# Kernel optimization log

Hardware: AMD Instinct MI355X
Metric: run time of the kernel (lower is better)

Reference implementation:

```python
import jax, jax.numpy as jnp
import numpy as np


def setup_inputs() -> dict:
    key = jax.random.key(0)
    k1, k2 = jax.random.split(key)
    B, L, D = 8, 4096, 1024
    hidden = jax.random.normal(k1, (B, L, D), dtype=jnp.float32)
    w1 = jax.random.normal(k2, (D // 2 + 1,), dtype=jnp.float32)
    return {"hidden": hidden, "w1": w1}


def reference(hidden, w1):
    # hidden: [B, L, D]; w1: [D//2+1]
    B, L, D = hidden.shape
    flat = hidden.reshape(-1, D)                 # [B*L, D]
    Xf1 = jnp.fft.rfft(flat, axis=1)             # [B*L, D//2+1] complex
    gate = jax.nn.softmax(w1, axis=0)[None, :]   # [1, D//2+1]
    t1 = jnp.fft.irfft(Xf1 * gate, n=D, axis=1)  # [B*L, D]
    return t1.reshape(B, L, D).astype(hidden.dtype)
```

## Files before the change

kernel.cpp:

```cpp
#include <hip/hip_runtime.h>


#define D_N 1024
#define TWO_PI_OVER_N 6.1359231515426636e-03f

__device__ __forceinline__ void cmulf(float& xr, float& xi, float wr, float wi) {
    float r = xr * wr - xi * wi;
    float i = xr * wi + xi * wr;
    xr = r; xi = i;
}

template <int S, bool INV>
__device__ __forceinline__ void fft_stage_store(
    int t,
    float ar, float ai, float br, float bi,
    float cr, float ci, float dr, float di,
    float* __restrict__ yr, float* __restrict__ yi)
{
    float apcr = ar + cr, apci = ai + ci;
    float amcr = ar - cr, amci = ai - ci;
    float bpdr = br + dr, bpdi = bi + di;
    float bmdr = br - dr, bmdi = bi - di;

    float y0r = apcr + bpdr, y0i = apci + bpdi;
    float y2r = apcr - bpdr, y2i = apci - bpdi;
    float y1r, y1i, y3r, y3i;
    if (!INV) {
        y1r = amcr + bmdi; y1i = amci - bmdr;
        y3r = amcr - bmdi; y3i = amci + bmdr;
    } else {
        y1r = amcr - bmdi; y1i = amci + bmdr;
        y3r = amcr + bmdi; y3i = amci - bmdr;
    }

    if (S < 256) {
        int j = t & ~(S - 1);
        float ang = (float)j * TWO_PI_OVER_N;
        float sn, cs;
        __sincosf(ang, &sn, &cs);
        float w1r = cs, w1i = INV ? sn : -sn;
        float w2r = w1r * w1r - w1i * w1i, w2i = 2.0f * w1r * w1i;
        float w3r = w2r * w1r - w2i * w1i, w3i = w2r * w1i + w2i * w1r;
        cmulf(y1r, y1i, w1r, w1i);
        cmulf(y2r, y2i, w2r, w2i);
        cmulf(y3r, y3i, w3r, w3i);
    }

    int bw = (t & (S - 1)) + ((t & ~(S - 1)) << 2);
    yr[bw        ] = y0r; yi[bw        ] = y0i;
    yr[bw +     S] = y1r; yi[bw +     S] = y1i;
    yr[bw + 2 * S] = y2r; yi[bw + 2 * S] = y2i;
    yr[bw + 3 * S] = y3r; yi[bw + 3 * S] = y3i;
}

__global__ __launch_bounds__(256)
void fft_filter_kernel(const float* __restrict__ x,
                       const float* __restrict__ G,
                       float* __restrict__ out)
{
    __shared__ float lAr[D_N], lAi[D_N], lBr[D_N], lBi[D_N];
    const int t = threadIdx.x;
    const size_t base = (size_t)blockIdx.x * D_N;

    {
        float x0 = x[base + t];
        float x1 = x[base + t + 256];
        float x2 = x[base + t + 512];
        float x3 = x[base + t + 768];
        fft_stage_store<1, false>(t, x0, 0.f, x1, 0.f, x2, 0.f, x3, 0.f, lBr, lBi);
    }
    __syncthreads();
    fft_stage_store<4, false>(t,
        lBr[t], lBi[t], lBr[t + 256], lBi[t + 256],
        lBr[t + 512], lBi[t + 512], lBr[t + 768], lBi[t + 768], lAr, lAi);
    __syncthreads();
    fft_stage_store<16, false>(t,
        lAr[t], lAi[t], lAr[t + 256], lAi[t + 256],
        lAr[t + 512], lAi[t + 512], lAr[t + 768], lAi[t + 768], lBr, lBi);
    __syncthreads();
    fft_stage_store<64, false>(t,
        lBr[t], lBi[t], lBr[t + 256], lBi[t + 256],
        lBr[t + 512], lBi[t + 512], lBr[t + 768], lBi[t + 768], lAr, lAi);
    __syncthreads();
    fft_stage_store<256, false>(t,
        lAr[t], lAi[t], lAr[t + 256], lAi[t + 256],
        lAr[t + 512], lAi[t + 512], lAr[t + 768], lAi[t + 768], lBr, lBi);
    __syncthreads();

    {
        float g0 = G[t], g1 = G[t + 256], g2 = G[t + 512], g3 = G[t + 768];
        fft_stage_store<1, true>(t,
            lBr[t] * g0, lBi[t] * g0,
            lBr[t + 256] * g1, lBi[t + 256] * g1,
            lBr[t + 512] * g2, lBi[t + 512] * g2,
            lBr[t + 768] * g3, lBi[t + 768] * g3, lAr, lAi);
    }
    __syncthreads();
    fft_stage_store<4, true>(t,
        lAr[t], lAi[t], lAr[t + 256], lAi[t + 256],
        lAr[t + 512], lAi[t + 512], lAr[t + 768], lAi[t + 768], lBr, lBi);
    __syncthreads();
    fft_stage_store<16, true>(t,
        lBr[t], lBi[t], lBr[t + 256], lBi[t + 256],
        lBr[t + 512], lBi[t + 512], lBr[t + 768], lBi[t + 768], lAr, lAi);
    __syncthreads();
    fft_stage_store<64, true>(t,
        lAr[t], lAi[t], lAr[t + 256], lAi[t + 256],
        lAr[t + 512], lAi[t + 512], lAr[t + 768], lAi[t + 768], lBr, lBi);
    __syncthreads();
    {
        float ar = lBr[t],       ai = lBi[t];
        float br = lBr[t + 256], bi = lBi[t + 256];
        float cr = lBr[t + 512], ci = lBi[t + 512];
        float dr = lBr[t + 768], di = lBi[t + 768];
        float apcr = ar + cr, amcr = ar - cr;
        float bpdr = br + dr, bmdi = bi - di;
        (void)ai; (void)ci;
        float y0r = apcr + bpdr;
        float y2r = apcr - bpdr;
        float y1r = amcr - bmdi;
        float y3r = amcr + bmdi;
        out[base + t      ] = y0r;
        out[base + t + 256] = y1r;
        out[base + t + 512] = y2r;
        out[base + t + 768] = y3r;
    }
}

__global__ void gate_kernel(const float* __restrict__ w1, float* __restrict__ G)
{
    __shared__ float red[1024];
    __shared__ float ex[513];
    const int t = threadIdx.x;

    float v = (t < 513) ? w1[t] : -1e30f;
    red[t] = v;
    __syncthreads();
    for (int off = 512; off > 0; off >>= 1) {
        if (t < off) red[t] = fmaxf(red[t], red[t + off]);
        __syncthreads();
    }
    float M = red[0];
    __syncthreads();

    float e = (t < 513) ? expf(w1[t] - M) : 0.0f;
    if (t < 513) ex[t] = e;
    red[t] = e;
    __syncthreads();
    for (int off = 512; off > 0; off >>= 1) {
        if (t < off) red[t] += red[t + off];
        __syncthreads();
    }
    float inv = 1.0f / (red[0] * 1024.0f);

    int k = (t <= 512) ? t : (1024 - t);
    G[t] = ex[k] * inv;
}

extern "C" void kernel_launch(void* const* d_in, const int* in_sizes, int n_in,
                              void* d_out, int out_size, void* d_ws, size_t ws_size,
                              hipStream_t stream)
{
    const float* hidden = (const float*)d_in[0];
    const float* w1     = (const float*)d_in[1];
    float* out = (float*)d_out;
    float* G   = (float*)d_ws;

    gate_kernel<<<1, 1024, 0, stream>>>(w1, G);

    const int rows = in_sizes[0] / D_N;
    fft_filter_kernel<<<rows, 256, 0, stream>>>(hidden, G, out);
}
```

Before: 270.5 us.

## Pack real rows as half-length complex FFT with radix-8 stages and precomputed twiddles

Replaces the 1024-point complex radix-4 FFT per row with a 512-point complex FFT that packs even and odd real samples as complex pairs. The gate is folded, together with the real-FFT split and merge, into one per-bin (P,q) multiplier applied between the forward and inverse passes. Stages become radix-8, so there are three passes each way instead of five, with XOR-swizzled shared memory to avoid bank conflicts and twiddle tables precomputed by the gate kernel. Each 256-thread block now handles four rows, one per 64-thread wave. This cuts arithmetic, LDS traffic and barriers, at the cost of more registers per thread and extra numerical reasoning in the folded gate.

```diff
diff --git a/kernel.cpp b/kernel.cpp
--- a/kernel.cpp
+++ b/kernel.cpp
@@ -1,133 +1,160 @@
 #include <hip/hip_runtime.h>
 
 
-#define D_N 1024
-#define TWO_PI_OVER_N 6.1359231515426636e-03f
-
-__device__ __forceinline__ void cmulf(float& xr, float& xi, float wr, float wi) {
-    float r = xr * wr - xi * wi;
-    float i = xr * wi + xi * wr;
-    xr = r; xi = i;
-}
-
-template <int S, bool INV>
-__device__ __forceinline__ void fft_stage_store(
-    int t,
-    float ar, float ai, float br, float bi,
-    float cr, float ci, float dr, float di,
-    float* __restrict__ yr, float* __restrict__ yi)
-{
-    float apcr = ar + cr, apci = ai + ci;
-    float amcr = ar - cr, amci = ai - ci;
-    float bpdr = br + dr, bpdi = bi + di;
-    float bmdr = br - dr, bmdi = bi - di;
-
-    float y0r = apcr + bpdr, y0i = apci + bpdi;
-    float y2r = apcr - bpdr, y2i = apci - bpdi;
-    float y1r, y1i, y3r, y3i;
+__device__ __forceinline__ int sw(int a) {
+    return a ^ (int)((((unsigned)a >> 6) * 9u) & 31u);
+}
+
+template <bool INV>
+__device__ __forceinline__ void bfly8(float* xr, float* xi)
+{
+    const float r2 = 0.70710678118654752f;
+    float t0r = xr[0] + xr[4], t0i = xi[0] + xi[4];
+    float t1r = xr[0] - xr[4], t1i = xi[0] - xi[4];
+    float t2r = xr[2] + xr[6], t2i = xi[2] + xi[6];
+    float t3r = xr[2] - xr[6], t3i = xi[2] - xi[6];
+    float e0r = t0r + t2r, e0i = t0i + t2i;
+    float e2r = t0r - t2r, e2i = t0i - t2i;
+    float e1r, e1i, e3r, e3i;
+    if (!INV) { e1r = t1r + t3i; e1i = t1i - t3r; e3r = t1r - t3i; e3i = t1i + t3r; }
+    else      { e1r = t1r - t3i; e1i = t1i + t3r; e3r = t1r + t3i; e3i = t1i - t3r; }
+    float s0r = xr[1] + xr[5], s0i = xi[1] + xi[5];
+    float s1r = xr[1] - xr[5], s1i = xi[1] - xi[5];
+    float s2r = xr[3] + xr[7], s2i = xi[3] + xi[7];
+    float s3r = xr[3] - xr[7], s3i = xi[3] - xi[7];
+    float o0r = s0r + s2r, o0i = s0i + s2i;
+    float o2r = s0r - s2r, o2i = s0i - s2i;
+    float o1r, o1i, o3r, o3i;
+    if (!INV) { o1r = s1r + s3i; o1i = s1i - s3r; o3r = s1r - s3i; o3i = s1i + s3r; }
+    else      { o1r = s1r - s3i; o1i = s1i + s3r; o3r = s1r + s3i; o3i = s1i - s3r; }
+    float p1r, p1i, p2r, p2i, p3r, p3i;
     if (!INV) {
-        y1r = amcr + bmdi; y1i = amci - bmdr;
-        y3r = amcr - bmdi; y3i = amci + bmdr;
+        p1r = (o1r + o1i) * r2;  p1i = (o1i - o1r) * r2;
+        p2r = o2i;               p2i = -o2r;
+        p3r = (o3i - o3r) * r2;  p3i = -(o3r + o3i) * r2;
     } else {
-        y1r = amcr - bmdi; y1i = amci + bmdr;
-        y3r = amcr + bmdi; y3i = amci - bmdr;
-    }
-
-    if (S < 256) {
-        int j = t & ~(S - 1);
-        float ang = (float)j * TWO_PI_OVER_N;
-        float sn, cs;
-        __sincosf(ang, &sn, &cs);
-        float w1r = cs, w1i = INV ? sn : -sn;
-        float w2r = w1r * w1r - w1i * w1i, w2i = 2.0f * w1r * w1i;
-        float w3r = w2r * w1r - w2i * w1i, w3i = w2r * w1i + w2i * w1r;
-        cmulf(y1r, y1i, w1r, w1i);
-        cmulf(y2r, y2i, w2r, w2i);
-        cmulf(y3r, y3i, w3r, w3i);
-    }
-
-    int bw = (t & (S - 1)) + ((t & ~(S - 1)) << 2);
-    yr[bw        ] = y0r; yi[bw        ] = y0i;
-    yr[bw +     S] = y1r; yi[bw +     S] = y1i;
-    yr[bw + 2 * S] = y2r; yi[bw + 2 * S] = y2i;
-    yr[bw + 3 * S] = y3r; yi[bw + 3 * S] = y3i;
+        p1r = (o1r - o1i) * r2;  p1i = (o1i + o1r) * r2;
+        p2r = -o2i;              p2i = o2r;
+        p3r = -(o3r + o3i) * r2; p3i = (o3r - o3i) * r2;
+    }
+    xr[0] = e0r + o0r; xi[0] = e0i + o0i;
+    xr[4] = e0r - o0r; xi[4] = e0i - o0i;
+    xr[1] = e1r + p1r; xi[1] = e1i + p1i;
+    xr[5] = e1r - p1r; xi[5] = e1i - p1i;
+    xr[2] = e2r + p2r; xi[2] = e2i + p2i;
+    xr[6] = e2r - p2r; xi[6] = e2i - p2i;
+    xr[3] = e3r + p3r; xi[3] = e3i + p3i;
+    xr[7] = e3r - p3r; xi[7] = e3i - p3i;
+}
+
+template <bool INV>
+__device__ __forceinline__ void tw_apply(float* xr, float* xi,
+                                         const float* c, const float* s)
+{
+#pragma unroll
+    for (int k = 1; k < 8; ++k) {
+        float r, i;
+        if (!INV) { r = xr[k] * c[k] + xi[k] * s[k]; i = xi[k] * c[k] - xr[k] * s[k]; }
+        else      { r = xr[k] * c[k] - xi[k] * s[k]; i = xi[k] * c[k] + xr[k] * s[k]; }
+        xr[k] = r; xi[k] = i;
+    }
+}
+
+template <int S>
+__device__ __forceinline__ void store_stage(int t, const float* xr, const float* xi,
+                                            float* dr, float* di)
+{
+    int base = (t & (S - 1)) + ((t & ~(S - 1)) << 3);
+#pragma unroll
+    for (int k = 0; k < 8; ++k) {
+        int idx = sw(base + k * S);
+        dr[idx] = xr[k]; di[idx] = xi[k];
+    }
+}
+
+__device__ __forceinline__ void load_stage(int t, float* xr, float* xi,
+                                           const float* dr, const float* di)
+{
+#pragma unroll
+    for (int k = 0; k < 8; ++k) {
+        int idx = sw(t + 64 * k);
+        xr[k] = dr[idx]; xi[k] = di[idx];
+    }
 }
 
 __global__ __launch_bounds__(256)
-void fft_filter_kernel(const float* __restrict__ x,
-                       const float* __restrict__ G,
-                       float* __restrict__ out)
-{
-    __shared__ float lAr[D_N], lAi[D_N], lBr[D_N], lBi[D_N];
-    const int t = threadIdx.x;
-    const size_t base = (size_t)blockIdx.x * D_N;
-
-    {
-        float x0 = x[base + t];
-        float x1 = x[base + t + 256];
-        float x2 = x[base + t + 512];
-        float x3 = x[base + t + 768];
-        fft_stage_store<1, false>(t, x0, 0.f, x1, 0.f, x2, 0.f, x3, 0.f, lBr, lBi);
-    }
-    __syncthreads();
-    fft_stage_store<4, false>(t,
-        lBr[t], lBi[t], lBr[t + 256], lBi[t + 256],
-        lBr[t + 512], lBi[t + 512], lBr[t + 768], lBi[t + 768], lAr, lAi);
-    __syncthreads();
-    fft_stage_store<16, false>(t,
-        lAr[t], lAi[t], lAr[t + 256], lAi[t + 256],
-        lAr[t + 512], lAi[t + 512], lAr[t + 768], lAi[t + 768], lBr, lBi);
-    __syncthreads();
-    fft_stage_store<64, false>(t,
-        lBr[t], lBi[t], lBr[t + 256], lBi[t + 256],
-        lBr[t + 512], lBi[t + 512], lBr[t + 768], lBi[t + 768], lAr, lAi);
-    __syncthreads();
-    fft_stage_store<256, false>(t,
-        lAr[t], lAi[t], lAr[t + 256], lAi[t + 256],
-        lAr[t + 512], lAi[t + 512], lAr[t + 768], lAi[t + 768], lBr, lBi);
-    __syncthreads();
-
-    {
-        float g0 = G[t], g1 = G[t + 256], g2 = G[t + 512], g3 = G[t + 768];
-        fft_stage_store<1, true>(t,
-            lBr[t] * g0, lBi[t] * g0,
-            lBr[t + 256] * g1, lBi[t + 256] * g1,
-            lBr[t + 512] * g2, lBi[t + 512] * g2,
-            lBr[t + 768] * g3, lBi[t + 768] * g3, lAr, lAi);
-    }
-    __syncthreads();
-    fft_stage_store<4, true>(t,
-        lAr[t], lAi[t], lAr[t + 256], lAi[t + 256],
-        lAr[t + 512], lAi[t + 512], lAr[t + 768], lAi[t + 768], lBr, lBi);
-    __syncthreads();
-    fft_stage_store<16, true>(t,
-        lBr[t], lBi[t], lBr[t + 256], lBi[t + 256],
-        lBr[t + 512], lBi[t + 512], lBr[t + 768], lBi[t + 768], lAr, lAi);
-    __syncthreads();
-    fft_stage_store<64, true>(t,
-        lAr[t], lAi[t], lAr[t + 256], lAi[t + 256],
-        lAr[t + 512], lAi[t + 512], lAr[t + 768], lAi[t + 768], lBr, lBi);
-    __syncthreads();
-    {
-        float ar = lBr[t],       ai = lBi[t];
-        float br = lBr[t + 256], bi = lBi[t + 256];
-        float cr = lBr[t + 512], ci = lBi[t + 512];
-        float dr = lBr[t + 768], di = lBi[t + 768];
-        float apcr = ar + cr, amcr = ar - cr;
-        float bpdr = br + dr, bmdi = bi - di;
-        (void)ai; (void)ci;
-        float y0r = apcr + bpdr;
-        float y2r = apcr - bpdr;
-        float y1r = amcr - bmdi;
-        float y3r = amcr + bmdi;
-        out[base + t      ] = y0r;
-        out[base + t + 256] = y1r;
-        out[base + t + 512] = y2r;
-        out[base + t + 768] = y3r;
-    }
-}
-
-__global__ void gate_kernel(const float* __restrict__ w1, float* __restrict__ G)
+void fv_kernel(const float2* __restrict__ x,
+               const float2* __restrict__ pq,
+               const float2* __restrict__ tw1,
+               const float2* __restrict__ tw8,
+               float2* __restrict__ out)
+{
+    __shared__ float Ar[4][512], Ai[4][512], Br[4][512], Bi[4][512];
+    const int tid = threadIdx.x;
+    const int r = tid >> 6;
+    const int t = tid & 63;
+    float* ar = Ar[r]; float* ai = Ai[r];
+    float* br = Br[r]; float* bi = Bi[r];
+    const size_t rowbase = ((size_t)blockIdx.x * 4 + r) * 512;
+
+    float c1[8], s1[8], c8[8], s8[8];
+#pragma unroll
+    for (int k = 1; k < 8; ++k) {
+        float2 w = tw1[(k - 1) * 64 + t];        c1[k] = w.x; s1[k] = w.y;
+        float2 v = tw8[(k - 1) * 8 + (t >> 3)];  c8[k] = v.x; s8[k] = v.y;
+    }
+
+    float zr[8], zi[8];
+
+#pragma unroll
+    for (int k = 0; k < 8; ++k) {
+        float2 v = x[rowbase + t + 64 * k];
+        zr[k] = v.x; zi[k] = v.y;
+    }
+    bfly8<false>(zr, zi);
+    tw_apply<false>(zr, zi, c1, s1);
+    store_stage<1>(t, zr, zi, ar, ai);
+
+    load_stage(t, zr, zi, ar, ai);
+    bfly8<false>(zr, zi);
+    tw_apply<false>(zr, zi, c8, s8);
+    store_stage<8>(t, zr, zi, br, bi);
+
+    load_stage(t, zr, zi, br, bi);
+    bfly8<false>(zr, zi);
+    store_stage<64>(t, zr, zi, ar, ai);
+
+#pragma unroll
+    for (int k = 0; k < 8; ++k) {
+        int idx = t + 64 * k;
+        int mir = (512 - idx) & 511;
+        float ur = ar[sw(idx)], ui = ai[sw(idx)];
+        float vr = ar[sw(mir)], vi = ai[sw(mir)];
+        float2 g = pq[idx];
+        zr[k] = g.x * ur + g.y * vi;
+        zi[k] = g.x * ui + g.y * vr;
+    }
+    bfly8<true>(zr, zi);
+    tw_apply<true>(zr, zi, c1, s1);
+    store_stage<1>(t, zr, zi, br, bi);
+
+    load_stage(t, zr, zi, br, bi);
+    bfly8<true>(zr, zi);
+    tw_apply<true>(zr, zi, c8, s8);
+    store_stage<8>(t, zr, zi, ar, ai);
+
+    load_stage(t, zr, zi, ar, ai);
+    bfly8<true>(zr, zi);
+#pragma unroll
+    for (int k = 0; k < 8; ++k) {
+        out[rowbase + t + 64 * k] = make_float2(zr[k], zi[k]);
+    }
+}
+
+__global__ void gate_kernel(const float* __restrict__ w1,
+                            float2* __restrict__ pq,
+                            float2* __restrict__ tw1,
+                            float2* __restrict__ tw8)
 {
     __shared__ float red[1024];
     __shared__ float ex[513];
@@ -151,23 +178,55 @@
         if (t < off) red[t] += red[t + off];
         __syncthreads();
     }
-    float inv = 1.0f / (red[0] * 1024.0f);
-
-    int k = (t <= 512) ? t : (1024 - t);
-    G[t] = ex[k] * inv;
+    float inv = 1.0f / red[0];
+    __syncthreads();
+
+    if (t < 512) {
+        float ga = ex[t] * inv;
+        float gb = ex[512 - t] * inv;
+        float gp = ga + gb, gm = ga - gb;
+        float th = (float)t * 3.06796157577128245e-03f;
+        th = (float)t * 6.13592315154256492e-03f;
+        float sn, cs;
+        __sincosf(th, &sn, &cs);
+        float P = 0.5f * (gp - gm * sn) * (1.0f / 512.0f);
+        float q = 0.5f * (gm * cs) * (1.0f / 512.0f);
+        pq[t] = make_float2(P, q);
+    }
+    if (t < 448) {
+        int k = (t >> 6) + 1;
+        int j = t & 63;
+        float th = (float)(j * k) * 1.22718463151036952e-02f;
+        float sn, cs;
+        sincosf(th, &sn, &cs);
+        tw1[t] = make_float2(cs, sn);
+    }
+    if (t < 56) {
+        int k = (t >> 3) + 1;
+        int p = t & 7;
+        float th = (float)(p * k) * 9.81747704246810387e-02f;
+        float sn, cs;
+        sincosf(th, &sn, &cs);
+        tw8[t] = make_float2(cs, sn);
+    }
 }
 
 extern "C" void kernel_launch(void* const* d_in, const int* in_sizes, int n_in,
                               void* d_out, int out_size, void* d_ws, size_t ws_size,
                               hipStream_t stream)
 {
-    const float* hidden = (const float*)d_in[0];
-    const float* w1     = (const float*)d_in[1];
-    float* out = (float*)d_out;
-    float* G   = (float*)d_ws;
-
-    gate_kernel<<<1, 1024, 0, stream>>>(w1, G);
-
-    const int rows = in_sizes[0] / D_N;
-    fft_filter_kernel<<<rows, 256, 0, stream>>>(hidden, G, out);
-}
+    (void)n_in; (void)out_size; (void)ws_size;
+    const float2* hidden = (const float2*)d_in[0];
+    const float*  w1     = (const float*)d_in[1];
+    float2* out = (float2*)d_out;
+
+    float2* pq  = (float2*)d_ws;
+    float2* tw1 = pq + 512;
+    float2* tw8 = tw1 + 448;
+
+    gate_kernel<<<1, 1024, 0, stream>>>(w1, pq, tw1, tw8);
+
+    const int rows   = in_sizes[0] / 1024;
+    const int blocks = rows / 4;
+    fv_kernel<<<blocks, 256, 0, stream>>>(hidden, pq, tw1, tw8, out);
+}
```

Result: faster. 236.1 us (-12.7%).
